# Performance work log

Hardware: AMD Instinct MI355X
Metric: run time of the kernel (lower is better)

## Reference

```python
import jax, jax.numpy as jnp
import numpy as np

N = 50000        # num_nodes = user + item
D = 128          # latdim
L = 3            # gnn layers
R = 16           # hyper_rank
E = 1600000      # nnz of ts_drp_adj


def setup_inputs() -> dict:
    key = jax.random.key(0)
    ks = jax.random.split(key, 13)
    s = 1.0 / np.sqrt(D)
    return {
        "adj_rows": jax.random.randint(ks[0], (E,), 0, N, dtype=jnp.int32),
        "adj_cols": jax.random.randint(ks[1], (E,), 0, N, dtype=jnp.int32),
        "adj_vals": jax.random.uniform(ks[2], (E,), jnp.float32) * 0.05,
        "node_feats": jax.random.normal(ks[3], (N, D), jnp.float32) * s,
        "gnn_W": jax.random.normal(ks[4], (L, D, D), jnp.float32) * s,
        "gnn_b": jax.random.normal(ks[5], (L, D), jnp.float32) * 0.01,
        "fc1_W": jax.random.normal(ks[6], (D, D), jnp.float32) * s,
        "fc1_b": jax.random.normal(ks[7], (D,), jnp.float32) * 0.01,
        "fcrow_W": jax.random.normal(ks[8], (N * R, D), jnp.float32) * s,
        "fcrow_b": jax.random.normal(ks[9], (N * R,), jnp.float32) * 0.01,
        "fccol_W": jax.random.normal(ks[10], (R * D, D), jnp.float32) * s,
        "fccol_b": jax.random.normal(ks[11], (R * D,), jnp.float32) * 0.01,
        "ini_embeds": jax.random.normal(ks[12], (N, D), jnp.float32) * s,
    }


def _spmm(rows, cols, vals, h):
    # out[i] = sum_{e: rows[e]==i} vals[e] * h[cols[e]]   -- sparse adj @ h
    return jax.ops.segment_sum(vals[:, None] * h[cols], rows, num_segments=N)


def reference(adj_rows, adj_cols, adj_vals, node_feats, gnn_W, gnn_b,
              fc1_W, fc1_b, fcrow_W, fcrow_b, fccol_W, fccol_b, ini_embeds):
    h = node_feats
    h_sum = h  # running sum of layer outputs (residual mean-pool)
    for l in range(L):
        agg = _spmm(adj_rows, adj_cols, adj_vals, h)           # (N, D)
        h = jax.nn.elu(agg @ gnn_W[l].T + gnn_b[l])            # linear + ELU
        h_sum = h_sum + h
    h_bar = h_sum / (L + 1)
    z = h_bar.mean(axis=0)                                     # (D,)
    # Hypernetwork: z -> low-rank W_u = W_row @ W_col
    hz = jax.nn.leaky_relu(z @ fc1_W.T + fc1_b, negative_slope=0.2)
    W_row = (hz @ fcrow_W.T + fcrow_b).reshape(N, R)
    W_col = (hz @ fccol_W.T + fccol_b).reshape(R, D)
    W_u = W_row @ W_col                                        # (N, D)
    tuned_emb = ini_embeds + W_u * ini_embeds
    return tuned_emb
```

## Files before the change

### kernel.cpp

```cpp
#include <hip/hip_runtime.h>
#include <hip/hip_bf16.h>
#include <math.h>

#define NN 50000
#define DD 128
#define LLAYERS 3
#define RR 16
#define EE 1600000

typedef unsigned int u32;

__device__ __forceinline__ float bflo(u32 u){ union{u32 i;float f;}a; a.i=u<<16; return a.f; }
__device__ __forceinline__ float bfhi(u32 u){ union{u32 i;float f;}a; a.i=u&0xffff0000u; return a.f; }
__device__ __forceinline__ u32 pack_bf2(float x, float y){
  union{float f;u32 i;}a,b; a.f=x; b.f=y;
  u32 xr = (a.i + 0x7fffu + ((a.i>>16)&1u)) >> 16;
  u32 yr = (b.i + 0x7fffu + ((b.i>>16)&1u)) & 0xffff0000u;
  return (xr & 0xffffu) | yr;
}

__global__ __launch_bounds__(256) void k_hist(const int* __restrict__ rows, int* __restrict__ cnt){
  int e = blockIdx.x*256 + threadIdx.x;
  if (e < EE) atomicAdd(&cnt[rows[e]], 1);
}

__global__ __launch_bounds__(256) void k_scanA(const int* __restrict__ cnt, int* __restrict__ bsum){
  __shared__ int s[256];
  int i = blockIdx.x*256 + threadIdx.x;
  int v = (i < NN) ? ((cnt[i]+7)&~7) : 0;
  s[threadIdx.x] = v; __syncthreads();
  for (int off=128; off>0; off>>=1){
    if (threadIdx.x < off) s[threadIdx.x] += s[threadIdx.x+off];
    __syncthreads();
  }
  if (threadIdx.x==0) bsum[blockIdx.x] = s[0];
}

__global__ __launch_bounds__(256) void k_scanB(int* bsum){
  __shared__ int s[256];
  int t = threadIdx.x;
  int v = bsum[t];
  s[t] = v; __syncthreads();
  for (int off=1; off<256; off<<=1){
    int x = (t>=off) ? s[t-off] : 0; __syncthreads();
    s[t] += x; __syncthreads();
  }
  bsum[t] = s[t] - v;
}

__global__ __launch_bounds__(256) void k_scanC(const int* __restrict__ cnt, const int* __restrict__ bsum,
                        int* __restrict__ row_ptr, int* __restrict__ cursor){
  __shared__ int s[256];
  int t = threadIdx.x; int i = blockIdx.x*256 + t;
  int v = (i<NN)?((cnt[i]+7)&~7):0;
  s[t]=v; __syncthreads();
  for (int off=1; off<256; off<<=1){
    int x=(t>=off)?s[t-off]:0; __syncthreads();
    s[t]+=x; __syncthreads();
  }
  if (i<NN){ int e = bsum[blockIdx.x] + s[t]-v; row_ptr[i]=e; cursor[i]=e; }
}

__global__ __launch_bounds__(256) void k_pad(const int* __restrict__ row_ptr, const int* __restrict__ cnt,
                                             int2* __restrict__ colval){
  int i = blockIdx.x*256 + threadIdx.x;
  if (i < NN){
    int b = row_ptr[i], n = cnt[i], np = (n+7)&~7;
    int2 z0; z0.x = 0; z0.y = 0;
    for (int p=b+n; p<b+np; ++p) colval[p] = z0;
    if (i == NN-1){
      for (int p=b+np; p<b+np+128; ++p) colval[p] = z0;
    }
  }
}

__global__ __launch_bounds__(256) void k_scatter(const int* __restrict__ rows, const int* __restrict__ cols,
                          const float* __restrict__ vals,
                          int* __restrict__ cursor, int2* __restrict__ colval){
  int e = blockIdx.x*256+threadIdx.x;
  if (e<EE){
    int r = rows[e];
    int p = atomicAdd(&cursor[r],1);
    int2 cv; cv.x = cols[e]; cv.y = __float_as_int(vals[e]);
    colval[p] = cv;
  }
}

__global__ __launch_bounds__(256) void k_init(const float4* __restrict__ nf, uint2* __restrict__ hbf,
                                              float* __restrict__ z){
  __shared__ float zp[128];
  int t = threadIdx.x;
  if (t < 128) zp[t] = 0.f;
  float a0=0.f,a1=0.f,a2=0.f,a3=0.f;
  for (int i = blockIdx.x*256 + t; i < NN*DD/4; i += gridDim.x*256){
    float4 v = nf[i];
    uint2 p; p.x = pack_bf2(v.x, v.y); p.y = pack_bf2(v.z, v.w);
    hbf[i] = p;
    a0 += v.x; a1 += v.y; a2 += v.z; a3 += v.w;
  }
  __syncthreads();
  int c = (t*4) & 127;
  atomicAdd(&zp[c],a0); atomicAdd(&zp[c+1],a1); atomicAdd(&zp[c+2],a2); atomicAdd(&zp[c+3],a3);
  __syncthreads();
  if (t < 128) atomicAdd(&z[((blockIdx.x&15)<<7) + t], zp[t]);
}

__global__ __launch_bounds__(256) void k_wT(const float* __restrict__ W, float* __restrict__ wT){
  int idx = blockIdx.x*256+threadIdx.x;
  int l = idx >> 14; int r = idx & 16383; int k = r >> 7; int j = r & 127;
  wT[(l<<14) + k*128 + j] = W[(l<<14) + j*128 + k];
}

#define FMA8(v, h)                                         \
  a0 = fmaf(v, bflo(h.x), a0); a1 = fmaf(v, bfhi(h.x), a1);\
  a2 = fmaf(v, bflo(h.y), a2); a3 = fmaf(v, bfhi(h.y), a3);\
  a4 = fmaf(v, bflo(h.z), a4); a5 = fmaf(v, bfhi(h.z), a5);\
  a6 = fmaf(v, bflo(h.w), a6); a7 = fmaf(v, bfhi(h.w), a7);

__global__ __launch_bounds__(256) void k_layer(const int* __restrict__ row_ptr, const int* __restrict__ cnt,
                       const int2* __restrict__ colval,
                       const u32* __restrict__ hin, const float* __restrict__ wTl,
                       const float* __restrict__ bl,
                       u32* __restrict__ hout, float* __restrict__ z, int last){
  __shared__ float a_s[16*128];
  __shared__ float zp[128];
  int t = threadIdx.x;
  if (t < 128) zp[t] = 0.f;
  int i0 = blockIdx.x * 16;
  int lane = t & 63;
  int wv = t >> 6;
  int sub = lane >> 4, k = lane & 15;

  for (int r = 0; r < 4; ++r){
    int row = i0 + wv*4 + r;
    int base = row_ptr[row], n = cnt[row];
    int iters = (n + 7) >> 3;
    const int2* cvp = colval + base + sub;
    float a0=0,a1=0,a2=0,a3=0,a4=0,a5=0,a6=0,a7=0;

    int2 c0a = cvp[0],  c0b = cvp[4];
    int2 c1a = cvp[8],  c1b = cvp[12];
    uint4 h0a = *(const uint4*)&hin[((size_t)(u32)c0a.x<<6) + (k<<2)];
    uint4 h0b = *(const uint4*)&hin[((size_t)(u32)c0b.x<<6) + (k<<2)];

    for (int it = 0; it < iters; ++it){
      int2 c2a = cvp[16], c2b = cvp[20];
      uint4 h1a = *(const uint4*)&hin[((size_t)(u32)c1a.x<<6) + (k<<2)];
      uint4 h1b = *(const uint4*)&hin[((size_t)(u32)c1b.x<<6) + (k<<2)];
      float v0 = __int_as_float(c0a.y);
      float v1 = __int_as_float(c0b.y);
      FMA8(v0, h0a);
      FMA8(v1, h0b);
      c0a = c1a; c0b = c1b; c1a = c2a; c1b = c2b;
      h0a = h1a; h0b = h1b;
      cvp += 8;
    }

    a0 += __shfl_xor(a0,16); a0 += __shfl_xor(a0,32);
    a1 += __shfl_xor(a1,16); a1 += __shfl_xor(a1,32);
    a2 += __shfl_xor(a2,16); a2 += __shfl_xor(a2,32);
    a3 += __shfl_xor(a3,16); a3 += __shfl_xor(a3,32);
    a4 += __shfl_xor(a4,16); a4 += __shfl_xor(a4,32);
    a5 += __shfl_xor(a5,16); a5 += __shfl_xor(a5,32);
    a6 += __shfl_xor(a6,16); a6 += __shfl_xor(a6,32);
    a7 += __shfl_xor(a7,16); a7 += __shfl_xor(a7,32);
    if (sub==0){
      float4 o0; o0.x=a0; o0.y=a1; o0.z=a2; o0.w=a3;
      float4 o1; o1.x=a4; o1.y=a5; o1.z=a6; o1.w=a7;
      *(float4*)&a_s[(wv*4+r)*128 + k*8] = o0;
      *(float4*)&a_s[(wv*4+r)*128 + k*8 + 4] = o1;
    }
  }
  __syncthreads();

  int jj = lane*2;
  float b0 = bl[jj], b1 = bl[jj+1];
  float acc[4][2];
  #pragma unroll
  for (int r=0;r<4;r++){ acc[r][0]=b0; acc[r][1]=b1; }
  #pragma unroll 4
  for (int kk=0;kk<128;kk++){
    float2 w2 = *(const float2*)&wTl[kk*128 + jj];
    #pragma unroll
    for (int r=0;r<4;r++){
      float a = a_s[(wv*4+r)*128 + kk];
      acc[r][0] = fmaf(a, w2.x, acc[r][0]);
      acc[r][1] = fmaf(a, w2.y, acc[r][1]);
    }
  }
  float zc0 = 0.f, zc1 = 0.f;
  #pragma unroll
  for (int r=0;r<4;r++){
    int row = i0 + wv*4 + r;
    float e0 = acc[r][0] > 0.f ? acc[r][0] : expm1f(acc[r][0]);
    float e1 = acc[r][1] > 0.f ? acc[r][1] : expm1f(acc[r][1]);
    zc0 += e0; zc1 += e1;
    if (!last)
      hout[(size_t)row*64 + (jj>>1)] = pack_bf2(e0, e1);
  }
  atomicAdd(&zp[jj], zc0); atomicAdd(&zp[jj+1], zc1);
  __syncthreads();
  if (t < 128) atomicAdd(&z[((blockIdx.x&15)<<7) + t], zp[t]);
}

__global__ __launch_bounds__(128) void k_hz(const float* __restrict__ z, const float* __restrict__ fc1W,
                     const float* __restrict__ fc1b, float* __restrict__ hz){
  __shared__ float zs[128];
  int j = threadIdx.x;
  float s = 0.f;
  #pragma unroll
  for (int q=0;q<16;q++) s += z[(q<<7) + j];
  zs[j] = s * (1.0f / (4.0f * (float)NN));
  __syncthreads();
  float acc = fc1b[j];
  const float* wr = &fc1W[j*128];
  #pragma unroll 8
  for (int k=0;k<128;k++)
    acc = fmaf(zs[k], wr[k], acc);
  hz[j] = acc >= 0.f ? acc : 0.2f*acc;
}

__global__ __launch_bounds__(256) void k_wcol(const float* __restrict__ hz, const float* __restrict__ W,
                       const float* __restrict__ b, float* __restrict__ wcol){
  __shared__ float hzs[128];
  int t = threadIdx.x;
  if (t < 128) hzs[t] = hz[t];
  __syncthreads();
  int m = blockIdx.x*256 + t;
  float acc = b[m];
  const float* wr = &W[(size_t)m*128];
  #pragma unroll 8
  for (int k=0;k<128;k++)
    acc = fmaf(hzs[k], wr[k], acc);
  wcol[m] = acc;
}

__global__ __launch_bounds__(256) void k_wrow(const float* __restrict__ hz, const float* __restrict__ W,
                       const float* __restrict__ b, float* __restrict__ wrow){
  int lane = threadIdx.x & 63;
  int sub = lane >> 5, k = lane & 31;
  float4 hk = *(const float4*)&hz[k*4];
  int wid = (blockIdx.x*blockDim.x + threadIdx.x) >> 6;
  int nw = (gridDim.x*blockDim.x) >> 6;
  const int NITER = NN*RR/2;
  for (int it = wid; it < NITER; it += nw){
    int row = it*2 + sub;
    float4 wv = *(const float4*)&W[(size_t)row*128 + k*4];
    float acc = wv.x*hk.x;
    acc = fmaf(wv.y, hk.y, acc);
    acc = fmaf(wv.z, hk.z, acc);
    acc = fmaf(wv.w, hk.w, acc);
    acc += __shfl_xor(acc,1); acc += __shfl_xor(acc,2);
    acc += __shfl_xor(acc,4); acc += __shfl_xor(acc,8);
    acc += __shfl_xor(acc,16);
    if (k==0) wrow[row] = acc + b[row];
  }
}

__global__ __launch_bounds__(256) void k_final(const float* __restrict__ ini, const float* __restrict__ wrow,
                        const float* __restrict__ wcol, float* __restrict__ out){
  __shared__ float wc[16*128];
  int t = threadIdx.x;
  ((float4*)wc)[t] = ((const float4*)wcol)[t];
  ((float4*)wc)[t+256] = ((const float4*)wcol)[t+256];
  __syncthreads();
  int gid = blockIdx.x*256 + t;
  int i = gid >> 5, k = gid & 31;
  float4 a; a.x=0.f; a.y=0.f; a.z=0.f; a.w=0.f;
  const float* wri = &wrow[(size_t)i*16];
  #pragma unroll
  for (int r=0;r<16;r++){
    float w = wri[r];
    const float4 c = *(const float4*)&wc[r*128 + k*4];
    a.x = fmaf(w, c.x, a.x); a.y = fmaf(w, c.y, a.y);
    a.z = fmaf(w, c.z, a.z); a.w = fmaf(w, c.w, a.w);
  }
  float4 e = *(const float4*)&ini[(size_t)i*128 + k*4];
  float4 o;
  o.x = e.x*(1.f+a.x); o.y = e.y*(1.f+a.y);
  o.z = e.z*(1.f+a.z); o.w = e.w*(1.f+a.w);
  *(float4*)&out[(size_t)i*128 + k*4] = o;
}

extern "C" void kernel_launch(void* const* d_in, const int* in_sizes, int n_in,
                              void* d_out, int out_size, void* d_ws, size_t ws_size,
                              hipStream_t stream) {
  const int* adj_rows = (const int*)d_in[0];
  const int* adj_cols = (const int*)d_in[1];
  const float* adj_vals = (const float*)d_in[2];
  const float* node_feats = (const float*)d_in[3];
  const float* gnn_W = (const float*)d_in[4];
  const float* gnn_b = (const float*)d_in[5];
  const float* fc1_W = (const float*)d_in[6];
  const float* fc1_b = (const float*)d_in[7];
  const float* fcrow_W = (const float*)d_in[8];
  const float* fcrow_b = (const float*)d_in[9];
  const float* fccol_W = (const float*)d_in[10];
  const float* fccol_b = (const float*)d_in[11];
  const float* ini = (const float*)d_in[12];
  float* out = (float*)d_out;

  char* w = (char*)d_ws;
  auto alloc = [&](size_t bytes)->void*{ void* p = (void*)w; w += (bytes + 255) & ~(size_t)255; return p; };
  u32*   hbf_a  = (u32*)  alloc((size_t)NN*DD*2);
  u32*   hbf_b  = (u32*)  alloc((size_t)NN*DD*2);
  int2*  colval = (int2*) alloc(((size_t)EE + 8*NN + 256)*8);
  int*   cnt    = (int*)  alloc((size_t)NN*4);
  int*   row_ptr= (int*)  alloc((size_t)NN*4);
  int*   cursor = (int*)  alloc((size_t)NN*4);
  int*   bsum   = (int*)  alloc(256*4);
  float* wT     = (float*)alloc(3*128*128*4);
  float* zb     = (float*)alloc(16*128*4);
  float* hzb    = (float*)alloc(128*4);
  float* wcolb  = (float*)alloc(2048*4);
  float* wrowb  = (float*)alloc((size_t)NN*RR*4);

  hipMemsetAsync(cnt, 0, NN*4, stream);
  hipMemsetAsync(zb, 0, 16*128*4, stream);

  k_hist<<<EE/256, 256, 0, stream>>>(adj_rows, cnt);
  k_scanA<<<256, 256, 0, stream>>>(cnt, bsum);
  k_scanB<<<1, 256, 0, stream>>>(bsum);
  k_scanC<<<256, 256, 0, stream>>>(cnt, bsum, row_ptr, cursor);
  k_pad<<<(NN+255)/256, 256, 0, stream>>>(row_ptr, cnt, colval);
  k_scatter<<<EE/256, 256, 0, stream>>>(adj_rows, adj_cols, adj_vals, cursor, colval);
  k_init<<<400, 256, 0, stream>>>((const float4*)node_feats, (uint2*)hbf_a, zb);
  k_wT<<<3*128*128/256, 256, 0, stream>>>(gnn_W, wT);

  const u32* hin = hbf_a; u32* hout = hbf_b;
  for (int l=0; l<LLAYERS; ++l){
    k_layer<<<NN/16, 256, 0, stream>>>(row_ptr, cnt, colval, hin, wT + l*16384,
                                       gnn_b + l*128, hout, zb, (l==LLAYERS-1) ? 1 : 0);
    const u32* tmp = hin; hin = hout; hout = (u32*)tmp;
  }

  k_hz<<<1, 128, 0, stream>>>(zb, fc1_W, fc1_b, hzb);
  k_wcol<<<8, 256, 0, stream>>>(hzb, fccol_W, fccol_b, wcolb);
  k_wrow<<<2048, 256, 0, stream>>>(hzb, fcrow_W, fcrow_b, wrowb);
  k_final<<<NN*32/256, 256, 0, stream>>>(ini, wrowb, wcolb, out);
}
```

Baseline: 1.094 ms.

## Fuse setup, hypernetwork and final kernels; stage layer weights in LDS

Several small kernels are merged to cut launch count and intermediate traffic. Row padding moves into the scan, the weight transpose into the init kernel, hz into the wcol kernel, and wrow into the final kernel so W_row never goes to global memory. The two memsets become one, and the per-layer dense matmul now stages weight chunks in shared memory. The costs are more syncthreads and extra LDS in the layer kernel, and the fused k_hzwcol recomputes hz redundantly in each of its 8 blocks.

```diff
diff --git a/kernel.cpp b/kernel.cpp
--- a/kernel.cpp
+++ b/kernel.cpp
@@ -49,27 +49,24 @@
 }
 
 __global__ __launch_bounds__(256) void k_scanC(const int* __restrict__ cnt, const int* __restrict__ bsum,
-                        int* __restrict__ row_ptr, int* __restrict__ cursor){
+                        int* __restrict__ row_ptr, int* __restrict__ cursor,
+                        int2* __restrict__ colval){
   __shared__ int s[256];
   int t = threadIdx.x; int i = blockIdx.x*256 + t;
-  int v = (i<NN)?((cnt[i]+7)&~7):0;
+  int n = (i<NN)?cnt[i]:0;
+  int v = (n+7)&~7;
   s[t]=v; __syncthreads();
   for (int off=1; off<256; off<<=1){
     int x=(t>=off)?s[t-off]:0; __syncthreads();
     s[t]+=x; __syncthreads();
   }
-  if (i<NN){ int e = bsum[blockIdx.x] + s[t]-v; row_ptr[i]=e; cursor[i]=e; }
-}
-
-__global__ __launch_bounds__(256) void k_pad(const int* __restrict__ row_ptr, const int* __restrict__ cnt,
-                                             int2* __restrict__ colval){
-  int i = blockIdx.x*256 + threadIdx.x;
-  if (i < NN){
-    int b = row_ptr[i], n = cnt[i], np = (n+7)&~7;
-    int2 z0; z0.x = 0; z0.y = 0;
-    for (int p=b+n; p<b+np; ++p) colval[p] = z0;
+  if (i<NN){
+    int e = bsum[blockIdx.x] + s[t]-v;
+    row_ptr[i]=e; cursor[i]=e;
+    int2 z0; z0.x=0; z0.y=0;
+    for (int p=e+n; p<e+v; ++p) colval[p] = z0;
     if (i == NN-1){
-      for (int p=b+np; p<b+np+128; ++p) colval[p] = z0;
+      for (int p=e+v; p<e+v+128; ++p) colval[p] = z0;
     }
   }
 }
@@ -86,11 +83,17 @@
   }
 }
 
-__global__ __launch_bounds__(256) void k_init(const float4* __restrict__ nf, uint2* __restrict__ hbf,
-                                              float* __restrict__ z){
+__global__ __launch_bounds__(256) void k_initwT(const float4* __restrict__ nf, uint2* __restrict__ hbf,
+                                                float* __restrict__ z,
+                                                const float* __restrict__ W, float* __restrict__ wT){
   __shared__ float zp[128];
   int t = threadIdx.x;
   if (t < 128) zp[t] = 0.f;
+  if (blockIdx.x < 192){
+    int idx = blockIdx.x*256+t;
+    int l = idx >> 14; int r = idx & 16383; int k = r >> 7; int j = r & 127;
+    wT[(l<<14) + k*128 + j] = W[(l<<14) + j*128 + k];
+  }
   float a0=0.f,a1=0.f,a2=0.f,a3=0.f;
   for (int i = blockIdx.x*256 + t; i < NN*DD/4; i += gridDim.x*256){
     float4 v = nf[i];
@@ -105,12 +108,6 @@
   if (t < 128) atomicAdd(&z[((blockIdx.x&15)<<7) + t], zp[t]);
 }
 
-__global__ __launch_bounds__(256) void k_wT(const float* __restrict__ W, float* __restrict__ wT){
-  int idx = blockIdx.x*256+threadIdx.x;
-  int l = idx >> 14; int r = idx & 16383; int k = r >> 7; int j = r & 127;
-  wT[(l<<14) + k*128 + j] = W[(l<<14) + j*128 + k];
-}
-
 #define FMA8(v, h)                                         \
   a0 = fmaf(v, bflo(h.x), a0); a1 = fmaf(v, bfhi(h.x), a1);\
   a2 = fmaf(v, bflo(h.y), a2); a3 = fmaf(v, bfhi(h.y), a3);\
@@ -123,6 +120,7 @@
                        const float* __restrict__ bl,
                        u32* __restrict__ hout, float* __restrict__ z, int last){
   __shared__ float a_s[16*128];
+  __shared__ float w_s[32*128];
   __shared__ float zp[128];
   int t = threadIdx.x;
   if (t < 128) zp[t] = 0.f;
@@ -178,15 +176,26 @@
   float acc[4][2];
   #pragma unroll
   for (int r=0;r<4;r++){ acc[r][0]=b0; acc[r][1]=b1; }
-  #pragma unroll 4
-  for (int kk=0;kk<128;kk++){
-    float2 w2 = *(const float2*)&wTl[kk*128 + jj];
-    #pragma unroll
-    for (int r=0;r<4;r++){
-      float a = a_s[(wv*4+r)*128 + kk];
-      acc[r][0] = fmaf(a, w2.x, acc[r][0]);
-      acc[r][1] = fmaf(a, w2.y, acc[r][1]);
+  for (int ch=0; ch<4; ++ch){
+    const float4* wsrc = (const float4*)(wTl + ch*32*128);
+    float4* wdst = (float4*)w_s;
+    wdst[t]     = wsrc[t];
+    wdst[t+256] = wsrc[t+256];
+    wdst[t+512] = wsrc[t+512];
+    wdst[t+768] = wsrc[t+768];
+    __syncthreads();
+    #pragma unroll 4
+    for (int kk=0;kk<32;kk++){
+      float2 w2 = *(const float2*)&w_s[kk*128 + jj];
+      int kg = ch*32 + kk;
+      #pragma unroll
+      for (int r=0;r<4;r++){
+        float a = a_s[(wv*4+r)*128 + kg];
+        acc[r][0] = fmaf(a, w2.x, acc[r][0]);
+        acc[r][1] = fmaf(a, w2.y, acc[r][1]);
+      }
     }
+    __syncthreads();
   }
   float zc0 = 0.f, zc1 = 0.f;
   #pragma unroll
@@ -203,83 +212,81 @@
   if (t < 128) atomicAdd(&z[((blockIdx.x&15)<<7) + t], zp[t]);
 }
 
-__global__ __launch_bounds__(128) void k_hz(const float* __restrict__ z, const float* __restrict__ fc1W,
-                     const float* __restrict__ fc1b, float* __restrict__ hz){
+__global__ __launch_bounds__(256) void k_hzwcol(const float* __restrict__ z, const float* __restrict__ fc1W,
+                     const float* __restrict__ fc1b, float* __restrict__ hzg,
+                     const float* __restrict__ Wc, const float* __restrict__ bc,
+                     float* __restrict__ wcol){
   __shared__ float zs[128];
-  int j = threadIdx.x;
-  float s = 0.f;
-  #pragma unroll
-  for (int q=0;q<16;q++) s += z[(q<<7) + j];
-  zs[j] = s * (1.0f / (4.0f * (float)NN));
-  __syncthreads();
-  float acc = fc1b[j];
-  const float* wr = &fc1W[j*128];
-  #pragma unroll 8
-  for (int k=0;k<128;k++)
-    acc = fmaf(zs[k], wr[k], acc);
-  hz[j] = acc >= 0.f ? acc : 0.2f*acc;
-}
-
-__global__ __launch_bounds__(256) void k_wcol(const float* __restrict__ hz, const float* __restrict__ W,
-                       const float* __restrict__ b, float* __restrict__ wcol){
   __shared__ float hzs[128];
   int t = threadIdx.x;
-  if (t < 128) hzs[t] = hz[t];
+  if (t < 128){
+    float s = 0.f;
+    #pragma unroll
+    for (int q=0;q<16;q++) s += z[(q<<7) + t];
+    zs[t] = s * (1.0f / (4.0f * (float)NN));
+  }
+  __syncthreads();
+  if (t < 128){
+    float acc = fc1b[t];
+    const float* wr = &fc1W[t*128];
+    #pragma unroll 8
+    for (int k=0;k<128;k++)
+      acc = fmaf(zs[k], wr[k], acc);
+    float h = acc >= 0.f ? acc : 0.2f*acc;
+    hzs[t] = h;
+    if (blockIdx.x==0) hzg[t] = h;
+  }
   __syncthreads();
   int m = blockIdx.x*256 + t;
-  float acc = b[m];
-  const float* wr = &W[(size_t)m*128];
+  float acc = bc[m];
+  const float* wr = &Wc[(size_t)m*128];
   #pragma unroll 8
   for (int k=0;k<128;k++)
     acc = fmaf(hzs[k], wr[k], acc);
   wcol[m] = acc;
 }
 
-__global__ __launch_bounds__(256) void k_wrow(const float* __restrict__ hz, const float* __restrict__ W,
-                       const float* __restrict__ b, float* __restrict__ wrow){
-  int lane = threadIdx.x & 63;
-  int sub = lane >> 5, k = lane & 31;
-  float4 hk = *(const float4*)&hz[k*4];
-  int wid = (blockIdx.x*blockDim.x + threadIdx.x) >> 6;
-  int nw = (gridDim.x*blockDim.x) >> 6;
-  const int NITER = NN*RR/2;
-  for (int it = wid; it < NITER; it += nw){
-    int row = it*2 + sub;
-    float4 wv = *(const float4*)&W[(size_t)row*128 + k*4];
-    float acc = wv.x*hk.x;
-    acc = fmaf(wv.y, hk.y, acc);
-    acc = fmaf(wv.z, hk.z, acc);
-    acc = fmaf(wv.w, hk.w, acc);
-    acc += __shfl_xor(acc,1); acc += __shfl_xor(acc,2);
-    acc += __shfl_xor(acc,4); acc += __shfl_xor(acc,8);
-    acc += __shfl_xor(acc,16);
-    if (k==0) wrow[row] = acc + b[row];
-  }
-}
-
-__global__ __launch_bounds__(256) void k_final(const float* __restrict__ ini, const float* __restrict__ wrow,
-                        const float* __restrict__ wcol, float* __restrict__ out){
+__global__ __launch_bounds__(256) void k_wrowfinal(const float* __restrict__ hz, const float* __restrict__ W,
+                        const float* __restrict__ b, const float* __restrict__ wcol,
+                        const float* __restrict__ ini, float* __restrict__ out){
   __shared__ float wc[16*128];
   int t = threadIdx.x;
   ((float4*)wc)[t] = ((const float4*)wcol)[t];
   ((float4*)wc)[t+256] = ((const float4*)wcol)[t+256];
   __syncthreads();
-  int gid = blockIdx.x*256 + t;
-  int i = gid >> 5, k = gid & 31;
-  float4 a; a.x=0.f; a.y=0.f; a.z=0.f; a.w=0.f;
-  const float* wri = &wrow[(size_t)i*16];
+  int lane = t & 63;
+  int i = (blockIdx.x*256 + t) >> 6;
+  int h = lane >> 5;
+  int kq = lane & 31;
+  float4 hzv = *(const float4*)&hz[kq*4];
+  const float4* wp = (const float4*)(W + (size_t)i*16*128);
+  const float* bp = b + (size_t)i*16;
+  float wr8[8];
   #pragma unroll
-  for (int r=0;r<16;r++){
-    float w = wri[r];
-    const float4 c = *(const float4*)&wc[r*128 + k*4];
-    a.x = fmaf(w, c.x, a.x); a.y = fmaf(w, c.y, a.y);
-    a.z = fmaf(w, c.z, a.z); a.w = fmaf(w, c.w, a.w);
-  }
-  float4 e = *(const float4*)&ini[(size_t)i*128 + k*4];
-  float4 o;
-  o.x = e.x*(1.f+a.x); o.y = e.y*(1.f+a.y);
-  o.z = e.z*(1.f+a.z); o.w = e.w*(1.f+a.w);
-  *(float4*)&out[(size_t)i*128 + k*4] = o;
+  for (int q=0;q<8;q++){
+    float4 wv = wp[q*64 + lane];
+    float p = wv.x*hzv.x;
+    p = fmaf(wv.y, hzv.y, p);
+    p = fmaf(wv.z, hzv.z, p);
+    p = fmaf(wv.w, hzv.w, p);
+    p += __shfl_xor(p,1); p += __shfl_xor(p,2); p += __shfl_xor(p,4);
+    p += __shfl_xor(p,8); p += __shfl_xor(p,16);
+    wr8[q] = p + bp[2*q + h];
+  }
+  int c = lane*2;
+  float a0=0.f, a1=0.f;
+  #pragma unroll
+  for (int q=0;q<8;q++){
+    float we = wr8[q];
+    float wo = __shfl_xor(wr8[q], 32);
+    const float2 cA = *(const float2*)&wc[(2*q+h)*128 + c];
+    const float2 cB = *(const float2*)&wc[(2*q+1-h)*128 + c];
+    a0 = fmaf(we, cA.x, a0); a1 = fmaf(we, cA.y, a1);
+    a0 = fmaf(wo, cB.x, a0); a1 = fmaf(wo, cB.y, a1);
+  }
+  float2 e = *(const float2*)&ini[(size_t)i*128 + c];
+  float2 o; o.x = e.x*(1.f+a0); o.y = e.y*(1.f+a1);
+  *(float2*)&out[(size_t)i*128 + c] = o;
 }
 
 extern "C" void kernel_launch(void* const* d_in, const int* in_sizes, int n_in,
@@ -302,30 +309,26 @@
 
   char* w = (char*)d_ws;
   auto alloc = [&](size_t bytes)->void*{ void* p = (void*)w; w += (bytes + 255) & ~(size_t)255; return p; };
+  int*   cnt    = (int*)  alloc((size_t)NN*4);
+  float* zb     = (float*)alloc(16*128*4);
   u32*   hbf_a  = (u32*)  alloc((size_t)NN*DD*2);
   u32*   hbf_b  = (u32*)  alloc((size_t)NN*DD*2);
   int2*  colval = (int2*) alloc(((size_t)EE + 8*NN + 256)*8);
-  int*   cnt    = (int*)  alloc((size_t)NN*4);
   int*   row_ptr= (int*)  alloc((size_t)NN*4);
   int*   cursor = (int*)  alloc((size_t)NN*4);
   int*   bsum   = (int*)  alloc(256*4);
   float* wT     = (float*)alloc(3*128*128*4);
-  float* zb     = (float*)alloc(16*128*4);
   float* hzb    = (float*)alloc(128*4);
   float* wcolb  = (float*)alloc(2048*4);
-  float* wrowb  = (float*)alloc((size_t)NN*RR*4);
-
-  hipMemsetAsync(cnt, 0, NN*4, stream);
-  hipMemsetAsync(zb, 0, 16*128*4, stream);
+
+  hipMemsetAsync(cnt, 0, ((NN*4 + 255) & ~(size_t)255) + 16*128*4, stream);
 
   k_hist<<<EE/256, 256, 0, stream>>>(adj_rows, cnt);
   k_scanA<<<256, 256, 0, stream>>>(cnt, bsum);
   k_scanB<<<1, 256, 0, stream>>>(bsum);
-  k_scanC<<<256, 256, 0, stream>>>(cnt, bsum, row_ptr, cursor);
-  k_pad<<<(NN+255)/256, 256, 0, stream>>>(row_ptr, cnt, colval);
+  k_scanC<<<256, 256, 0, stream>>>(cnt, bsum, row_ptr, cursor, colval);
   k_scatter<<<EE/256, 256, 0, stream>>>(adj_rows, adj_cols, adj_vals, cursor, colval);
-  k_init<<<400, 256, 0, stream>>>((const float4*)node_feats, (uint2*)hbf_a, zb);
-  k_wT<<<3*128*128/256, 256, 0, stream>>>(gnn_W, wT);
+  k_initwT<<<400, 256, 0, stream>>>((const float4*)node_feats, (uint2*)hbf_a, zb, gnn_W, wT);
 
   const u32* hin = hbf_a; u32* hout = hbf_b;
   for (int l=0; l<LLAYERS; ++l){
@@ -334,8 +337,6 @@
     const u32* tmp = hin; hin = hout; hout = (u32*)tmp;
   }
 
-  k_hz<<<1, 128, 0, stream>>>(zb, fc1_W, fc1_b, hzb);
-  k_wcol<<<8, 256, 0, stream>>>(hzb, fccol_W, fccol_b, wcolb);
-  k_wrow<<<2048, 256, 0, stream>>>(hzb, fcrow_W, fcrow_b, wrowb);
-  k_final<<<NN*32/256, 256, 0, stream>>>(ini, wrowb, wcolb, out);
-}
+  k_hzwcol<<<8, 256, 0, stream>>>(zb, fc1_W, fc1_b, hzb, fccol_W, fccol_b, wcolb);
+  k_wrowfinal<<<NN/4, 256, 0, stream>>>(hzb, fcrow_W, fcrow_b, wcolb, ini, out);
+}
```

Measured after the change: 1.033 ms. -5.5%, faster.
